# Performance work log

Hardware: AMD Instinct MI355X
Metric: run time of the kernel (lower is better)

Reference implementation:

```python
import jax, jax.numpy as jnp
import numpy as np

EPS = 1e-12  # F.normalize eps


def setup_inputs() -> dict:
    key = jax.random.key(0)
    k1, k2 = jax.random.split(key)
    B, T, C, E = 4, 4096, 2048, 64
    return {
        "hidden_states": jax.random.normal(k1, (B, T, C), dtype=jnp.float32),
        "sim_matrix": jax.random.normal(k2, (C, E), dtype=jnp.float32),
        "gates": jnp.zeros((E,), dtype=jnp.float32),
        "min_experts": 2,
    }


def reference(hidden_states, sim_matrix, gates, min_experts):
    b, t, c = hidden_states.shape
    h = hidden_states.reshape(b * t, c)
    # L2-normalize tokens (dim=-1) and expert columns (dim=0)
    hn = h / jnp.maximum(jnp.linalg.norm(h, axis=-1, keepdims=True), EPS)
    wn = sim_matrix / jnp.maximum(jnp.linalg.norm(sim_matrix, axis=0, keepdims=True), EPS)
    logits = hn @ wn - jax.nn.sigmoid(gates)          # [N, E]
    gated = jax.nn.relu(logits)
    # STE threshold (forward: hard 0/1 indicator)
    ind = (gated > 0).astype(gated.dtype)
    mask = gated + jax.lax.stop_gradient(ind - gated)
    # fallback: rows with no active expert get top-min_experts of raw logits
    inactive = jnp.sum(ind, axis=1) == 0              # [N]
    _, topk_idx = jax.lax.top_k(logits, min_experts)  # [N, k]
    n = mask.shape[0]
    fallback = jnp.zeros((n, logits.shape[1]), dtype=bool).at[
        jnp.arange(n)[:, None], topk_idx].set(True)
    put = inactive[:, None] & fallback                # positions overwritten with 1.0
    mask = jnp.where(put, jnp.asarray(1.0, mask.dtype), mask)
    masked = jnp.where(mask > 0, gated, -jnp.inf)
    routing_weights = jax.nn.softmax(masked, axis=-1)
    return routing_weights, logits, mask
```

## Files before the change

kernel.cpp:

```cpp
#include <hip/hip_runtime.h>
#include <math.h>

#define CDIM 2048
#define EDIM 64
#define BM   32
#define NITW 16
#define PREPB 32

#define SCALE_H 1024.0f
#define SCALE_W 4096.0f
#define INV_SCALE (1.0f / 4194304.0f)

typedef float    f32x16 __attribute__((ext_vector_type(16)));
typedef float    f32x4  __attribute__((ext_vector_type(4)));
typedef _Float16 f16x8  __attribute__((ext_vector_type(8)));
typedef __fp16   cvt_t  __attribute__((ext_vector_type(2)));

__global__ void prep_w(const float* __restrict__ W,
                       unsigned short* __restrict__ bfrag,
                       float* __restrict__ pnw) {
    __shared__ float tile[64][65];
    __shared__ float part[4][64];
    const int t = threadIdx.x;
    const int c0 = blockIdx.x * 64;
#pragma unroll
    for (int p = 0; p < 4; ++p) {
        int r = (t >> 4) + p * 16;
        float4 v = *reinterpret_cast<const float4*>(W + (size_t)(c0 + r) * EDIM + (t & 15) * 4);
        tile[r][(t & 15) * 4 + 0] = v.x;
        tile[r][(t & 15) * 4 + 1] = v.y;
        tile[r][(t & 15) * 4 + 2] = v.z;
        tile[r][(t & 15) * 4 + 3] = v.w;
    }
    __syncthreads();
    {
        int g = t >> 6, e = t & 63;
        float s = 0.f;
#pragma unroll
        for (int j = 0; j < 16; ++j) { float v = tile[g * 16 + j][e]; s += v * v; }
        part[g][e] = s;
    }
    __syncthreads();
    if (t < 64) pnw[blockIdx.x * EDIM + t] = part[0][t] + part[1][t] + part[2][t] + part[3][t];
    const int nt = t >> 7, hl = (t >> 6) & 1, lane = t & 63;
    const int e = nt * 32 + (lane & 31);
    const int kb = (lane >> 5) * 8;
#pragma unroll
    for (int s = 0; s < 4; ++s) {
        int kl = s * 16 + kb;
        unsigned int wds[4];
#pragma unroll
        for (int pj = 0; pj < 4; ++pj) {
            float v0 = tile[kl + 2 * pj][e] * SCALE_W;
            float v1 = tile[kl + 2 * pj + 1][e] * SCALE_W;
            cvt_t hh = __builtin_amdgcn_cvt_pkrtz(v0, v1);
            if (hl) {
                cvt_t ll = __builtin_amdgcn_cvt_pkrtz(v0 - (float)hh[0], v1 - (float)hh[1]);
                wds[pj] = __builtin_bit_cast(unsigned int, ll);
            } else {
                wds[pj] = __builtin_bit_cast(unsigned int, hh);
            }
        }
        size_t off = ((size_t)(blockIdx.x * 4 + s)) * 2048 + (size_t)nt * 1024 + (size_t)hl * 512 + (size_t)lane * 8;
        *reinterpret_cast<uint4*>(bfrag + off) = make_uint4(wds[0], wds[1], wds[2], wds[3]);
    }
}

template<int BUF>
__device__ __forceinline__ void stageA(int it, int w, int l, int row0,
    const float* __restrict__ H, float (&aS)[4][2][32][32]) {
#pragma unroll
    for (int J = 0; J < 4; ++J) {
        const int row_ = 8 * J + (l >> 3);
        const float* src = H + (size_t)(row0 + row_) * CDIM + w * 512 + it * 32
                         + (((l & 7) ^ (row_ & 7)) << 2);
        __builtin_amdgcn_global_load_lds(
            (const __attribute__((address_space(1))) unsigned int*)src,
            (__attribute__((address_space(3))) unsigned int*)&aS[w][BUF][8 * J][0], 16, 0, 0);
    }
}

__device__ __forceinline__ void loadB(int it, int w, int l,
    const unsigned short* __restrict__ bfrag, uint4 (&b)[8]) {
    const int kc0 = w * 32 + it * 2;
#pragma unroll
    for (int kc2 = 0; kc2 < 2; ++kc2)
#pragma unroll
        for (int nt = 0; nt < 2; ++nt)
#pragma unroll
            for (int hl = 0; hl < 2; ++hl)
                b[kc2 * 4 + nt * 2 + hl] = *reinterpret_cast<const uint4*>(
                    bfrag + (size_t)(kc0 + kc2) * 2048 + nt * 1024 + hl * 512 + (size_t)l * 8);
}

template<int BUF, bool LAST>
__device__ __forceinline__ void kstep(int it, int w, int l, int row0,
    const float* __restrict__ H, const unsigned short* __restrict__ bfrag,
    float (&aS)[4][2][32][32], f32x16 (&acc)[2], float& nacc) {
    uint4 bcur[8];
    loadB(it, w, l, bfrag, bcur);
    if (!LAST) stageA<BUF ^ 1>(it + 1, w, l, row0, H, aS);
    __builtin_amdgcn_sched_barrier(0);
    if (LAST) { asm volatile("s_waitcnt vmcnt(0)" ::: "memory"); }
    else      { asm volatile("s_waitcnt vmcnt(4)" ::: "memory"); }
    __builtin_amdgcn_sched_barrier(0);

    const int r = l & 31, kg = l >> 5;
#pragma unroll
    for (int kc2 = 0; kc2 < 2; ++kc2) {
        const int c0 = kc2 * 4 + kg * 2;
        f32x4 a0 = *reinterpret_cast<const f32x4*>(&aS[w][BUF][r][((c0)     ^ (r & 7)) * 4]);
        f32x4 a1 = *reinterpret_cast<const f32x4*>(&aS[w][BUF][r][((c0 + 1) ^ (r & 7)) * 4]);
        float f0 = a0[0], f1 = a0[1], f2 = a0[2], f3 = a0[3];
        float f4 = a1[0], f5 = a1[1], f6 = a1[2], f7 = a1[3];
        nacc += f0*f0 + f1*f1 + f2*f2 + f3*f3 + f4*f4 + f5*f5 + f6*f6 + f7*f7;
        float s0 = f0*SCALE_H, s1 = f1*SCALE_H, s2 = f2*SCALE_H, s3 = f3*SCALE_H;
        float s4 = f4*SCALE_H, s5 = f5*SCALE_H, s6 = f6*SCALE_H, s7 = f7*SCALE_H;
        cvt_t h0 = __builtin_amdgcn_cvt_pkrtz(s0, s1);
        cvt_t h1 = __builtin_amdgcn_cvt_pkrtz(s2, s3);
        cvt_t h2 = __builtin_amdgcn_cvt_pkrtz(s4, s5);
        cvt_t h3 = __builtin_amdgcn_cvt_pkrtz(s6, s7);
        cvt_t l0 = __builtin_amdgcn_cvt_pkrtz(s0 - (float)h0[0], s1 - (float)h0[1]);
        cvt_t l1 = __builtin_amdgcn_cvt_pkrtz(s2 - (float)h1[0], s3 - (float)h1[1]);
        cvt_t l2 = __builtin_amdgcn_cvt_pkrtz(s4 - (float)h2[0], s5 - (float)h2[1]);
        cvt_t l3 = __builtin_amdgcn_cvt_pkrtz(s6 - (float)h3[0], s7 - (float)h3[1]);
        f16x8 ah = __builtin_bit_cast(f16x8, make_uint4(
            __builtin_bit_cast(unsigned int, h0), __builtin_bit_cast(unsigned int, h1),
            __builtin_bit_cast(unsigned int, h2), __builtin_bit_cast(unsigned int, h3)));
        f16x8 al = __builtin_bit_cast(f16x8, make_uint4(
            __builtin_bit_cast(unsigned int, l0), __builtin_bit_cast(unsigned int, l1),
            __builtin_bit_cast(unsigned int, l2), __builtin_bit_cast(unsigned int, l3)));
        f16x8 bh0 = __builtin_bit_cast(f16x8, bcur[kc2 * 4 + 0]);
        f16x8 bl0 = __builtin_bit_cast(f16x8, bcur[kc2 * 4 + 1]);
        f16x8 bh1 = __builtin_bit_cast(f16x8, bcur[kc2 * 4 + 2]);
        f16x8 bl1 = __builtin_bit_cast(f16x8, bcur[kc2 * 4 + 3]);
        acc[0] = __builtin_amdgcn_mfma_f32_32x32x16_f16(ah, bh0, acc[0], 0, 0, 0);
        acc[1] = __builtin_amdgcn_mfma_f32_32x32x16_f16(ah, bh1, acc[1], 0, 0, 0);
        acc[0] = __builtin_amdgcn_mfma_f32_32x32x16_f16(ah, bl0, acc[0], 0, 0, 0);
        acc[1] = __builtin_amdgcn_mfma_f32_32x32x16_f16(ah, bl1, acc[1], 0, 0, 0);
        acc[0] = __builtin_amdgcn_mfma_f32_32x32x16_f16(al, bh0, acc[0], 0, 0, 0);
        acc[1] = __builtin_amdgcn_mfma_f32_32x32x16_f16(al, bh1, acc[1], 0, 0, 0);
    }
}

__launch_bounds__(256, 3)
__global__ void gating_main(const float* __restrict__ H,
                            const unsigned short* __restrict__ bfrag,
                            const float* __restrict__ pnw,
                            const float* __restrict__ gates,
                            float* __restrict__ out_rw,
                            float* __restrict__ out_lg,
                            float* __restrict__ out_mk) {
    __shared__ float aS[4][2][32][32];
    __shared__ float normred[4][32];
    __shared__ float invw_s[64], sig_s[64];

    const int t = threadIdx.x;
    const int w = t >> 6, l = t & 63;
    const int row0 = blockIdx.x * BM;
    const int kg = l >> 5, arow = l & 31;

    f32x16 acc[2];
#pragma unroll
    for (int a = 0; a < 2; ++a)
#pragma unroll
        for (int i = 0; i < 16; ++i) acc[a][i] = 0.f;
    float nacc = 0.f;

    stageA<0>(0, w, l, row0, H, aS);
#pragma unroll
    for (int ot = 0; ot < 7; ++ot) {
        kstep<0, false>(2 * ot,     w, l, row0, H, bfrag, aS, acc, nacc);
        kstep<1, false>(2 * ot + 1, w, l, row0, H, bfrag, aS, acc, nacc);
    }
    kstep<0, false>(14, w, l, row0, H, bfrag, aS, acc, nacc);
    kstep<1, true >(15, w, l, row0, H, bfrag, aS, acc, nacc);

    __syncthreads();

    float* redp = &aS[0][0][0][0];
#pragma unroll
    for (int nt = 0; nt < 2; ++nt)
#pragma unroll
        for (int r = 0; r < 16; ++r) {
            int row = (r & 3) + 8 * (r >> 2) + 4 * kg;
            redp[((size_t)w * 32 + row) * 64 + nt * 32 + arow] = acc[nt][r];
        }
    nacc += __shfl_xor(nacc, 32);
    if (l < 32) normred[w][l] = nacc;
    if (t < 64) {
        float s2 = 0.f;
#pragma unroll
        for (int b = 0; b < PREPB; ++b) s2 += pnw[b * EDIM + t];
        invw_s[t] = 1.f / fmaxf(sqrtf(s2), 1e-12f);
        sig_s[t] = 1.f / (1.f + __expf(-gates[t]));
    }
    __syncthreads();

    const int rr = t >> 3, e0 = (t & 7) * 8;
    const int orow = row0 + rr;
    float nh = normred[0][rr] + normred[1][rr] + normred[2][rr] + normred[3][rr];
    float invh = INV_SCALE / fmaxf(sqrtf(nh), 1e-12f);
    float lg[8];
#pragma unroll
    for (int k2 = 0; k2 < 8; ++k2) {
        int ee = e0 + k2;
        float s = redp[(0 * 32 + rr) * 64 + ee] + redp[(1 * 32 + rr) * 64 + ee]
                + redp[(2 * 32 + rr) * 64 + ee] + redp[(3 * 32 + rr) * 64 + ee];
        lg[k2] = s * invh * invw_s[ee] - sig_s[ee];
    }
    float* plg = out_lg + (size_t)orow * EDIM + e0;
    *reinterpret_cast<float4*>(plg)     = make_float4(lg[0], lg[1], lg[2], lg[3]);
    *reinterpret_cast<float4*>(plg + 4) = make_float4(lg[4], lg[5], lg[6], lg[7]);

    float v1 = -INFINITY, v2 = -INFINITY;
    int i1 = 0x7fffffff, i2 = 0x7fffffff, cnt = 0;
#pragma unroll
    for (int j = 0; j < 8; ++j) {
        int ee = e0 + j;
        float v = lg[j];
        cnt += (v > 0.f) ? 1 : 0;
        if (v > v1) { v2 = v1; i2 = i1; v1 = v; i1 = ee; }
        else if (v > v2) { v2 = v; i2 = ee; }
    }
#pragma unroll
    for (int st = 1; st <= 4; st <<= 1) {
        float w1 = __shfl_xor(v1, st);
        int   j1 = __shfl_xor(i1, st);
        float wv2 = __shfl_xor(v2, st);
        int   j2 = __shfl_xor(i2, st);
        int   cc = __shfl_xor(cnt, st);
        cnt += cc;
        bool g = (w1 > v1) || (w1 == v1 && j1 < i1);
        if (g) {
            bool g2 = (v1 > wv2) || (v1 == wv2 && i1 < j2);
            float nv2 = g2 ? v1 : wv2;
            int   ni2 = g2 ? i1 : j2;
            v1 = w1; i1 = j1; v2 = nv2; i2 = ni2;
        } else {
            bool g2 = (w1 > v2) || (w1 == v2 && j1 < i2);
            if (g2) { v2 = w1; i2 = j1; }
        }
    }
    bool act = cnt > 0;
    float rmax = act ? v1 : 0.f;
    float xs[8], ms[8];
    float wsum = 0.f;
#pragma unroll
    for (int j = 0; j < 8; ++j) {
        int ee = e0 + j;
        float lv = lg[j];
        float x, m;
        if (act) {
            bool sel = lv > 0.f;
            m = sel ? 1.f : 0.f;
            x = sel ? __expf(lv - rmax) : 0.f;
        } else {
            bool sel = (ee == i1) || (ee == i2);
            m = sel ? 1.f : 0.f;
            x = m;
        }
        xs[j] = x; ms[j] = m; wsum += x;
    }
    wsum += __shfl_xor(wsum, 1);
    wsum += __shfl_xor(wsum, 2);
    wsum += __shfl_xor(wsum, 4);
    float invd = 1.f / wsum;
    float* prw = out_rw + (size_t)orow * EDIM + e0;
    float* pmk = out_mk + (size_t)orow * EDIM + e0;
    *reinterpret_cast<float4*>(prw)     = make_float4(xs[0]*invd, xs[1]*invd, xs[2]*invd, xs[3]*invd);
    *reinterpret_cast<float4*>(prw + 4) = make_float4(xs[4]*invd, xs[5]*invd, xs[6]*invd, xs[7]*invd);
    *reinterpret_cast<float4*>(pmk)     = make_float4(ms[0], ms[1], ms[2], ms[3]);
    *reinterpret_cast<float4*>(pmk + 4) = make_float4(ms[4], ms[5], ms[6], ms[7]);
}

extern "C" void kernel_launch(void* const* d_in, const int* in_sizes, int n_in,
                              void* d_out, int out_size, void* d_ws, size_t ws_size,
                              hipStream_t stream) {
    const float* H     = (const float*)d_in[0];
    const float* Wm    = (const float*)d_in[1];
    const float* gates = (const float*)d_in[2];
    const int ntok = in_sizes[0] / CDIM;

    unsigned short* bfrag = (unsigned short*)d_ws;
    float* pnw = (float*)(bfrag + (size_t)262144);

    float* out_rw = (float*)d_out;
    float* out_lg = out_rw + (size_t)ntok * EDIM;
    float* out_mk = out_lg + (size_t)ntok * EDIM;

    hipLaunchKernelGGL(prep_w, dim3(PREPB), dim3(256), 0, stream, Wm, bfrag, pnw);
    hipLaunchKernelGGL(gating_main, dim3(ntok / BM), dim3(256), 0, stream,
                       H, bfrag, pnw, gates, out_rw, out_lg, out_mk);
}
```

Measured before the change: 36.06 us.

## Split K reduction across eight waves per block instead of four

Doubles the block to 512 threads so each of eight waves handles a 256-column K slice in 8 steps. The cross-wave reduction and epilogue are remapped to 16 threads per row with 4 experts each. The aim is shorter per-wave serial K loops and more waves in flight. It doubles LDS per block and tightens the register budget via the launch bounds, which may cause spills.

New measurement: 42.74 us. 1.19x slower.

```diff
diff --git a/kernel.cpp b/kernel.cpp
--- a/kernel.cpp
+++ b/kernel.cpp
@@ -4,7 +4,7 @@
 #define CDIM 2048
 #define EDIM 64
 #define BM   32
-#define NITW 16
+#define NITW 8
 #define PREPB 32
 
 #define SCALE_H 1024.0f
@@ -68,11 +68,11 @@
 
 template<int BUF>
 __device__ __forceinline__ void stageA(int it, int w, int l, int row0,
-    const float* __restrict__ H, float (&aS)[4][2][32][32]) {
+    const float* __restrict__ H, float (&aS)[8][2][32][32]) {
 #pragma unroll
     for (int J = 0; J < 4; ++J) {
         const int row_ = 8 * J + (l >> 3);
-        const float* src = H + (size_t)(row0 + row_) * CDIM + w * 512 + it * 32
+        const float* src = H + (size_t)(row0 + row_) * CDIM + w * 256 + it * 32
                          + (((l & 7) ^ (row_ & 7)) << 2);
         __builtin_amdgcn_global_load_lds(
             (const __attribute__((address_space(1))) unsigned int*)src,
@@ -82,7 +82,7 @@
 
 __device__ __forceinline__ void loadB(int it, int w, int l,
     const unsigned short* __restrict__ bfrag, uint4 (&b)[8]) {
-    const int kc0 = w * 32 + it * 2;
+    const int kc0 = w * 16 + it * 2;
 #pragma unroll
     for (int kc2 = 0; kc2 < 2; ++kc2)
 #pragma unroll
@@ -96,7 +96,7 @@
 template<int BUF, bool LAST>
 __device__ __forceinline__ void kstep(int it, int w, int l, int row0,
     const float* __restrict__ H, const unsigned short* __restrict__ bfrag,
-    float (&aS)[4][2][32][32], f32x16 (&acc)[2], float& nacc) {
+    float (&aS)[8][2][32][32], f32x16 (&acc)[2], float& nacc) {
     uint4 bcur[8];
     loadB(it, w, l, bfrag, bcur);
     if (!LAST) stageA<BUF ^ 1>(it + 1, w, l, row0, H, aS);
@@ -143,7 +143,7 @@
     }
 }
 
-__launch_bounds__(256, 3)
+__launch_bounds__(512, 4)
 __global__ void gating_main(const float* __restrict__ H,
                             const unsigned short* __restrict__ bfrag,
                             const float* __restrict__ pnw,
@@ -151,8 +151,8 @@
                             float* __restrict__ out_rw,
                             float* __restrict__ out_lg,
                             float* __restrict__ out_mk) {
-    __shared__ float aS[4][2][32][32];
-    __shared__ float normred[4][32];
+    __shared__ float aS[8][2][32][32];
+    __shared__ float normred[8][32];
     __shared__ float invw_s[64], sig_s[64];
 
     const int t = threadIdx.x;
@@ -168,13 +168,14 @@
     float nacc = 0.f;
 
     stageA<0>(0, w, l, row0, H, aS);
-#pragma unroll
-    for (int ot = 0; ot < 7; ++ot) {
-        kstep<0, false>(2 * ot,     w, l, row0, H, bfrag, aS, acc, nacc);
-        kstep<1, false>(2 * ot + 1, w, l, row0, H, bfrag, aS, acc, nacc);
-    }
-    kstep<0, false>(14, w, l, row0, H, bfrag, aS, acc, nacc);
-    kstep<1, true >(15, w, l, row0, H, bfrag, aS, acc, nacc);
+    kstep<0, false>(0, w, l, row0, H, bfrag, aS, acc, nacc);
+    kstep<1, false>(1, w, l, row0, H, bfrag, aS, acc, nacc);
+    kstep<0, false>(2, w, l, row0, H, bfrag, aS, acc, nacc);
+    kstep<1, false>(3, w, l, row0, H, bfrag, aS, acc, nacc);
+    kstep<0, false>(4, w, l, row0, H, bfrag, aS, acc, nacc);
+    kstep<1, false>(5, w, l, row0, H, bfrag, aS, acc, nacc);
+    kstep<0, false>(6, w, l, row0, H, bfrag, aS, acc, nacc);
+    kstep<1, true >(7, w, l, row0, H, bfrag, aS, acc, nacc);
 
     __syncthreads();
 
@@ -197,26 +198,28 @@
     }
     __syncthreads();
 
-    const int rr = t >> 3, e0 = (t & 7) * 8;
+    const int rr = t >> 4, e0 = (t & 15) * 4;
     const int orow = row0 + rr;
-    float nh = normred[0][rr] + normred[1][rr] + normred[2][rr] + normred[3][rr];
+    float nh = 0.f;
+#pragma unroll
+    for (int s = 0; s < 8; ++s) nh += normred[s][rr];
     float invh = INV_SCALE / fmaxf(sqrtf(nh), 1e-12f);
-    float lg[8];
-#pragma unroll
-    for (int k2 = 0; k2 < 8; ++k2) {
+    float lg[4];
+#pragma unroll
+    for (int k2 = 0; k2 < 4; ++k2) {
         int ee = e0 + k2;
-        float s = redp[(0 * 32 + rr) * 64 + ee] + redp[(1 * 32 + rr) * 64 + ee]
-                + redp[(2 * 32 + rr) * 64 + ee] + redp[(3 * 32 + rr) * 64 + ee];
+        float s = 0.f;
+#pragma unroll
+        for (int sw = 0; sw < 8; ++sw) s += redp[((size_t)sw * 32 + rr) * 64 + ee];
         lg[k2] = s * invh * invw_s[ee] - sig_s[ee];
     }
-    float* plg = out_lg + (size_t)orow * EDIM + e0;
-    *reinterpret_cast<float4*>(plg)     = make_float4(lg[0], lg[1], lg[2], lg[3]);
-    *reinterpret_cast<float4*>(plg + 4) = make_float4(lg[4], lg[5], lg[6], lg[7]);
+    *reinterpret_cast<float4*>(out_lg + (size_t)orow * EDIM + e0) =
+        make_float4(lg[0], lg[1], lg[2], lg[3]);
 
     float v1 = -INFINITY, v2 = -INFINITY;
     int i1 = 0x7fffffff, i2 = 0x7fffffff, cnt = 0;
 #pragma unroll
-    for (int j = 0; j < 8; ++j) {
+    for (int j = 0; j < 4; ++j) {
         int ee = e0 + j;
         float v = lg[j];
         cnt += (v > 0.f) ? 1 : 0;
@@ -224,7 +227,7 @@
         else if (v > v2) { v2 = v; i2 = ee; }
     }
 #pragma unroll
-    for (int st = 1; st <= 4; st <<= 1) {
+    for (int st = 1; st <= 8; st <<= 1) {
         float w1 = __shfl_xor(v1, st);
         int   j1 = __shfl_xor(i1, st);
         float wv2 = __shfl_xor(v2, st);
@@ -244,10 +247,10 @@
     }
     bool act = cnt > 0;
     float rmax = act ? v1 : 0.f;
-    float xs[8], ms[8];
+    float xs[4], ms[4];
     float wsum = 0.f;
 #pragma unroll
-    for (int j = 0; j < 8; ++j) {
+    for (int j = 0; j < 4; ++j) {
         int ee = e0 + j;
         float lv = lg[j];
         float x, m;
@@ -265,13 +268,12 @@
     wsum += __shfl_xor(wsum, 1);
     wsum += __shfl_xor(wsum, 2);
     wsum += __shfl_xor(wsum, 4);
+    wsum += __shfl_xor(wsum, 8);
     float invd = 1.f / wsum;
-    float* prw = out_rw + (size_t)orow * EDIM + e0;
-    float* pmk = out_mk + (size_t)orow * EDIM + e0;
-    *reinterpret_cast<float4*>(prw)     = make_float4(xs[0]*invd, xs[1]*invd, xs[2]*invd, xs[3]*invd);
-    *reinterpret_cast<float4*>(prw + 4) = make_float4(xs[4]*invd, xs[5]*invd, xs[6]*invd, xs[7]*invd);
-    *reinterpret_cast<float4*>(pmk)     = make_float4(ms[0], ms[1], ms[2], ms[3]);
-    *reinterpret_cast<float4*>(pmk + 4) = make_float4(ms[4], ms[5], ms[6], ms[7]);
+    *reinterpret_cast<float4*>(out_rw + (size_t)orow * EDIM + e0) =
+        make_float4(xs[0] * invd, xs[1] * invd, xs[2] * invd, xs[3] * invd);
+    *reinterpret_cast<float4*>(out_mk + (size_t)orow * EDIM + e0) =
+        make_float4(ms[0], ms[1], ms[2], ms[3]);
 }
 
 extern "C" void kernel_launch(void* const* d_in, const int* in_sizes, int n_in,
@@ -290,6 +292,6 @@
     float* out_mk = out_lg + (size_t)ntok * EDIM;
 
     hipLaunchKernelGGL(prep_w, dim3(PREPB), dim3(256), 0, stream, Wm, bfrag, pnw);
-    hipLaunchKernelGGL(gating_main, dim3(ntok / BM), dim3(256), 0, stream,
+    hipLaunchKernelGGL(gating_main, dim3(ntok / BM), dim3(512), 0, stream,
                        H, bfrag, pnw, gates, out_rw, out_lg, out_mk);
 }
```

## Split K dimension across two blocks with separate finalize kernel

Applied to the files above, without the earlier changes.

Splits the 2048-wide reduction into two halves handled by separate blocks (grid y=2), doubling the block count from 512 to 1024. Partial dot products and partial token norms are written to workspace, and a new finalize kernel sums them and applies normalization, gating, top-2 fallback and softmax. This aims to raise occupancy and latency hiding on a memory-bound GEMV-like kernel. In exchange it adds a third kernel launch and an extra round trip of partial results through global memory.

After: 51.33 us. +42.3%, slower.

```diff
diff --git a/kernel.cpp b/kernel.cpp
--- a/kernel.cpp
+++ b/kernel.cpp
@@ -4,7 +4,7 @@
 #define CDIM 2048
 #define EDIM 64
 #define BM   32
-#define NITW 16
+#define NITW 8
 #define PREPB 32
 
 #define SCALE_H 1024.0f
@@ -67,12 +67,12 @@
 }
 
 template<int BUF>
-__device__ __forceinline__ void stageA(int it, int w, int l, int row0,
+__device__ __forceinline__ void stageA(int it, int w, int l, int row0, int kbase,
     const float* __restrict__ H, float (&aS)[4][2][32][32]) {
 #pragma unroll
     for (int J = 0; J < 4; ++J) {
         const int row_ = 8 * J + (l >> 3);
-        const float* src = H + (size_t)(row0 + row_) * CDIM + w * 512 + it * 32
+        const float* src = H + (size_t)(row0 + row_) * CDIM + kbase + w * 256 + it * 32
                          + (((l & 7) ^ (row_ & 7)) << 2);
         __builtin_amdgcn_global_load_lds(
             (const __attribute__((address_space(1))) unsigned int*)src,
@@ -80,9 +80,9 @@
     }
 }
 
-__device__ __forceinline__ void loadB(int it, int w, int l,
+__device__ __forceinline__ void loadB(int it, int w, int l, int kcbase,
     const unsigned short* __restrict__ bfrag, uint4 (&b)[8]) {
-    const int kc0 = w * 32 + it * 2;
+    const int kc0 = kcbase + w * 16 + it * 2;
 #pragma unroll
     for (int kc2 = 0; kc2 < 2; ++kc2)
 #pragma unroll
@@ -94,12 +94,12 @@
 }
 
 template<int BUF, bool LAST>
-__device__ __forceinline__ void kstep(int it, int w, int l, int row0,
+__device__ __forceinline__ void kstep(int it, int w, int l, int row0, int kbase,
     const float* __restrict__ H, const unsigned short* __restrict__ bfrag,
     float (&aS)[4][2][32][32], f32x16 (&acc)[2], float& nacc) {
     uint4 bcur[8];
-    loadB(it, w, l, bfrag, bcur);
-    if (!LAST) stageA<BUF ^ 1>(it + 1, w, l, row0, H, aS);
+    loadB(it, w, l, kbase >> 4, bfrag, bcur);
+    if (!LAST) stageA<BUF ^ 1>(it + 1, w, l, row0, kbase, H, aS);
     __builtin_amdgcn_sched_barrier(0);
     if (LAST) { asm volatile("s_waitcnt vmcnt(0)" ::: "memory"); }
     else      { asm volatile("s_waitcnt vmcnt(4)" ::: "memory"); }
@@ -144,20 +144,18 @@
 }
 
 __launch_bounds__(256, 3)
-__global__ void gating_main(const float* __restrict__ H,
-                            const unsigned short* __restrict__ bfrag,
-                            const float* __restrict__ pnw,
-                            const float* __restrict__ gates,
-                            float* __restrict__ out_rw,
-                            float* __restrict__ out_lg,
-                            float* __restrict__ out_mk) {
+__global__ void gating_splitk(const float* __restrict__ H,
+                              const unsigned short* __restrict__ bfrag,
+                              float* __restrict__ pdot,
+                              float* __restrict__ pnorm) {
     __shared__ float aS[4][2][32][32];
     __shared__ float normred[4][32];
-    __shared__ float invw_s[64], sig_s[64];
 
     const int t = threadIdx.x;
     const int w = t >> 6, l = t & 63;
     const int row0 = blockIdx.x * BM;
+    const int ky = blockIdx.y;
+    const int kbase = ky * 1024;
     const int kg = l >> 5, arow = l & 31;
 
     f32x16 acc[2];
@@ -167,14 +165,15 @@
         for (int i = 0; i < 16; ++i) acc[a][i] = 0.f;
     float nacc = 0.f;
 
-    stageA<0>(0, w, l, row0, H, aS);
-#pragma unroll
-    for (int ot = 0; ot < 7; ++ot) {
-        kstep<0, false>(2 * ot,     w, l, row0, H, bfrag, aS, acc, nacc);
-        kstep<1, false>(2 * ot + 1, w, l, row0, H, bfrag, aS, acc, nacc);
-    }
-    kstep<0, false>(14, w, l, row0, H, bfrag, aS, acc, nacc);
-    kstep<1, true >(15, w, l, row0, H, bfrag, aS, acc, nacc);
+    stageA<0>(0, w, l, row0, kbase, H, aS);
+    kstep<0, false>(0, w, l, row0, kbase, H, bfrag, aS, acc, nacc);
+    kstep<1, false>(1, w, l, row0, kbase, H, bfrag, aS, acc, nacc);
+    kstep<0, false>(2, w, l, row0, kbase, H, bfrag, aS, acc, nacc);
+    kstep<1, false>(3, w, l, row0, kbase, H, bfrag, aS, acc, nacc);
+    kstep<0, false>(4, w, l, row0, kbase, H, bfrag, aS, acc, nacc);
+    kstep<1, false>(5, w, l, row0, kbase, H, bfrag, aS, acc, nacc);
+    kstep<0, false>(6, w, l, row0, kbase, H, bfrag, aS, acc, nacc);
+    kstep<1, true >(7, w, l, row0, kbase, H, bfrag, aS, acc, nacc);
 
     __syncthreads();
 
@@ -188,6 +187,33 @@
         }
     nacc += __shfl_xor(nacc, 32);
     if (l < 32) normred[w][l] = nacc;
+    __syncthreads();
+
+    const int rr = t >> 3, e0 = (t & 7) * 8;
+    float s[8];
+#pragma unroll
+    for (int j = 0; j < 8; ++j) {
+        int e = e0 + j;
+        s[j] = redp[(0 * 32 + rr) * 64 + e] + redp[(1 * 32 + rr) * 64 + e]
+             + redp[(2 * 32 + rr) * 64 + e] + redp[(3 * 32 + rr) * 64 + e];
+    }
+    float* pd = pdot + (((size_t)ky * 512 + blockIdx.x) * 32 + rr) * 64 + e0;
+    *reinterpret_cast<float4*>(pd)     = make_float4(s[0], s[1], s[2], s[3]);
+    *reinterpret_cast<float4*>(pd + 4) = make_float4(s[4], s[5], s[6], s[7]);
+    if ((t & 7) == 0)
+        pnorm[((size_t)ky * 512 + blockIdx.x) * 32 + rr] =
+            normred[0][rr] + normred[1][rr] + normred[2][rr] + normred[3][rr];
+}
+
+__global__ void gating_fin(const float* __restrict__ pdot,
+                           const float* __restrict__ pnorm,
+                           const float* __restrict__ pnw,
+                           const float* __restrict__ gates,
+                           float* __restrict__ out_rw,
+                           float* __restrict__ out_lg,
+                           float* __restrict__ out_mk) {
+    __shared__ float invw_s[64], sig_s[64];
+    const int t = threadIdx.x;
     if (t < 64) {
         float s2 = 0.f;
 #pragma unroll
@@ -198,16 +224,25 @@
     __syncthreads();
 
     const int rr = t >> 3, e0 = (t & 7) * 8;
-    const int orow = row0 + rr;
-    float nh = normred[0][rr] + normred[1][rr] + normred[2][rr] + normred[3][rr];
+    const int orow = blockIdx.x * 32 + rr;
+    float nh = pnorm[((size_t)0 * 512 + blockIdx.x) * 32 + rr]
+             + pnorm[((size_t)1 * 512 + blockIdx.x) * 32 + rr];
     float invh = INV_SCALE / fmaxf(sqrtf(nh), 1e-12f);
+
+    const float* pd0 = pdot + (((size_t)0 * 512 + blockIdx.x) * 32 + rr) * 64 + e0;
+    const float* pd1 = pdot + (((size_t)1 * 512 + blockIdx.x) * 32 + rr) * 64 + e0;
     float lg[8];
 #pragma unroll
-    for (int k2 = 0; k2 < 8; ++k2) {
-        int ee = e0 + k2;
-        float s = redp[(0 * 32 + rr) * 64 + ee] + redp[(1 * 32 + rr) * 64 + ee]
-                + redp[(2 * 32 + rr) * 64 + ee] + redp[(3 * 32 + rr) * 64 + ee];
-        lg[k2] = s * invh * invw_s[ee] - sig_s[ee];
+    for (int i = 0; i < 2; ++i) {
+        float4 a = *reinterpret_cast<const float4*>(pd0 + i * 4);
+        float4 b = *reinterpret_cast<const float4*>(pd1 + i * 4);
+        lg[i*4+0] = a.x + b.x; lg[i*4+1] = a.y + b.y;
+        lg[i*4+2] = a.z + b.z; lg[i*4+3] = a.w + b.w;
+    }
+#pragma unroll
+    for (int j = 0; j < 8; ++j) {
+        int ee = e0 + j;
+        lg[j] = lg[j] * invh * invw_s[ee] - sig_s[ee];
     }
     float* plg = out_lg + (size_t)orow * EDIM + e0;
     *reinterpret_cast<float4*>(plg)     = make_float4(lg[0], lg[1], lg[2], lg[3]);
@@ -281,15 +316,20 @@
     const float* Wm    = (const float*)d_in[1];
     const float* gates = (const float*)d_in[2];
     const int ntok = in_sizes[0] / CDIM;
+    const int nmb  = ntok / BM;
 
     unsigned short* bfrag = (unsigned short*)d_ws;
-    float* pnw = (float*)(bfrag + (size_t)262144);
+    float* pnw   = (float*)(bfrag + (size_t)262144);
+    float* pdot  = pnw + 32 * 64;
+    float* pnorm = pdot + (size_t)2 * 512 * 32 * 64;
 
     float* out_rw = (float*)d_out;
     float* out_lg = out_rw + (size_t)ntok * EDIM;
     float* out_mk = out_lg + (size_t)ntok * EDIM;
 
     hipLaunchKernelGGL(prep_w, dim3(PREPB), dim3(256), 0, stream, Wm, bfrag, pnw);
-    hipLaunchKernelGGL(gating_main, dim3(ntok / BM), dim3(256), 0, stream,
-                       H, bfrag, pnw, gates, out_rw, out_lg, out_mk);
-}
+    hipLaunchKernelGGL(gating_splitk, dim3(nmb, 2), dim3(256), 0, stream,
+                       H, bfrag, pdot, pnorm);
+    hipLaunchKernelGGL(gating_fin, dim3(nmb), dim3(256), 0, stream,
+                       pdot, pnorm, pnw, gates, out_rw, out_lg, out_mk);
+}
```
